# Optimization experiments

Measured on AMD Instinct MI355X. Metric: run time of the kernel, lower is better.

Reference implementation:

```python
import jax, jax.numpy as jnp
import numpy as np

N = 50000
E = 800000
IN_DIM = 128
HID = 64
HEADS = 4
OUT = 64


def _bn(x, g, b, eps=1e-5):
    # BatchNorm1d with batch statistics (biased var), as in train-mode normalization
    mu = x.mean(0)
    var = ((x - mu) ** 2).mean(0)
    return (x - mu) * jax.lax.rsqrt(var + eps) * g + b


def _gat(x, W, a_src, a_dst, bias, src, dst, heads, dim, concat):
    # PyG GATConv: h = xW; e_ij = LeakyReLU(a_src.h_j + a_dst.h_i); softmax over incoming edges of i
    n = x.shape[0]
    h = (x @ W).reshape(n, heads, dim)            # [N,H,D]
    es = (h * a_src).sum(-1)                      # [N,H]
    ed = (h * a_dst).sum(-1)                      # [N,H]
    e = jax.nn.leaky_relu(es[src] + ed[dst], 0.2)  # [E,H]
    emax = jax.ops.segment_max(e, dst, num_segments=n)
    w = jnp.exp(e - emax[dst])
    denom = jax.ops.segment_sum(w, dst, num_segments=n)
    alpha = w / (denom[dst] + 1e-16)              # [E,H]
    out = jax.ops.segment_sum(h[src] * alpha[:, :, None], dst, num_segments=n)  # [N,H,D]
    out = out.reshape(n, heads * dim) if concat else out.mean(axis=1)
    return out + bias


def _gcn(x, W, bias, src, dst):
    # PyG GCNConv with self-loops (already appended): D^{-1/2} A D^{-1/2} x W
    n = x.shape[0]
    h = x @ W
    deg = jax.ops.segment_sum(jnp.ones(src.shape[0], h.dtype), dst, num_segments=n)
    dinv = jax.lax.rsqrt(jnp.maximum(deg, 1e-12))
    norm = dinv[src] * dinv[dst]                  # [E]
    return jax.ops.segment_sum(h[src] * norm[:, None], dst, num_segments=n) + bias


def setup_inputs() -> dict:
    key = jax.random.key(0)
    ks = jax.random.split(key, 16)
    s = 0.1
    inp = {
        "x": jax.random.normal(ks[0], (N, IN_DIM), jnp.float32),
        "edge_index": jax.random.randint(ks[1], (2, E), 0, N, jnp.int64 if jax.config.jax_enable_x64 else jnp.int32),
        "edge_attr": jax.random.normal(ks[2], (E,), jnp.float32),
        # GAT layer 1
        "W1": jax.random.normal(ks[3], (IN_DIM, HEADS * HID), jnp.float32) * s,
        "att_src1": jax.random.normal(ks[4], (HEADS, HID), jnp.float32) * s,
        "att_dst1": jax.random.normal(ks[5], (HEADS, HID), jnp.float32) * s,
        "b1": jnp.zeros((HEADS * HID,), jnp.float32),
        "g1": jnp.ones((HEADS * HID,), jnp.float32),
        "beta1": jnp.zeros((HEADS * HID,), jnp.float32),
        # GCN
        "Wg": jax.random.normal(ks[6], (HEADS * HID, HID), jnp.float32) * s,
        "bg": jnp.zeros((HID,), jnp.float32),
        "g2": jnp.ones((HID,), jnp.float32),
        "beta2": jnp.zeros((HID,), jnp.float32),
        # GAT layer 2 (heads=1, concat=False)
        "W2": jax.random.normal(ks[7], (HID, OUT), jnp.float32) * s,
        "att_src2": jax.random.normal(ks[8], (1, OUT), jnp.float32) * s,
        "att_dst2": jax.random.normal(ks[9], (1, OUT), jnp.float32) * s,
        "b2": jnp.zeros((OUT,), jnp.float32),
        "g3": jnp.ones((OUT,), jnp.float32),
        "beta3": jnp.zeros((OUT,), jnp.float32),
        # projector
        "Wp1": jax.random.normal(ks[10], (OUT, 128), jnp.float32) * s,
        "bp1": jnp.zeros((128,), jnp.float32),
        "Wp2": jax.random.normal(ks[11], (128, 64), jnp.float32) * s,
        "bp2": jnp.zeros((64,), jnp.float32),
    }
    return inp


def reference(x, edge_index, edge_attr, W1, att_src1, att_dst1, b1, g1, beta1,
              Wg, bg, g2, beta2, W2, att_src2, att_dst2, b2, g3, beta3,
              Wp1, bp1, Wp2, bp2):
    # edge_attr is ignored by GATConv when edge_dim is None (PyG behavior)
    loop = jnp.arange(N, dtype=edge_index.dtype)
    src = jnp.concatenate([edge_index[0], loop])  # self-loops appended
    dst = jnp.concatenate([edge_index[1], loop])
    h = _gat(x, W1, att_src1, att_dst1, b1, src, dst, HEADS, HID, True)
    h = jax.nn.elu(_bn(h, g1, beta1))
    h = _gcn(h, Wg, bg, src, dst)
    h = jax.nn.relu(_bn(h, g2, beta2))
    h = _gat(h, W2, att_src2, att_dst2, b2, src, dst, 1, OUT, False)
    h = jax.nn.elu(_bn(h, g3, beta3))
    return jax.nn.relu(h @ Wp1 + bp1) @ Wp2 + bp2
```

## Files before the change

### kernel.cpp

```cpp
#include <hip/hip_runtime.h>
#include <math.h>

#define NN 50000
#define EE 800000
#define E2 850000
#define SCB 196
#define GXL 391

typedef __attribute__((ext_vector_type(8))) short short8;
typedef __attribute__((ext_vector_type(4))) float float4v;

__device__ __forceinline__ float bf2f(unsigned short u) {
  return __uint_as_float(((unsigned int)u) << 16);
}
__device__ __forceinline__ unsigned short f2bf(float f) {
  unsigned int x = __float_as_uint(f);
  unsigned int r = (x + 0x7fffu + ((x >> 16) & 1u)) >> 16;
  return (unsigned short)r;
}

__device__ __forceinline__ float leaky(float x) { return x > 0.f ? x : 0.2f * x; }

__device__ __forceinline__ int edge_src(const int* ei, int e) {
  return (e < EE) ? ei[e] : (e - EE);
}
__device__ __forceinline__ int edge_dst(const int* ei, int e) {
  return (e < EE) ? ei[EE + e] : (e - EE);
}

__global__ void k_deg(const int* __restrict__ ei, int* __restrict__ deg) {
  int e = blockIdx.x * blockDim.x + threadIdx.x;
  if (e < E2) atomicAdd(&deg[edge_dst(ei, e)], 1);
}

__global__ __launch_bounds__(256) void k_scan1(const int* __restrict__ deg,
                                               int* __restrict__ partial) {
  __shared__ int sd[256];
  int i = blockIdx.x * 256 + threadIdx.x;
  sd[threadIdx.x] = (i < NN) ? deg[i] : 0;
  __syncthreads();
  for (int off = 128; off > 0; off >>= 1) {
    if (threadIdx.x < off) sd[threadIdx.x] += sd[threadIdx.x + off];
    __syncthreads();
  }
  if (threadIdx.x == 0) partial[blockIdx.x] = sd[0];
}

__global__ __launch_bounds__(256) void k_scan3(const int* __restrict__ deg,
                                               const int* __restrict__ partial,
                                               int* __restrict__ rowptr,
                                               int* __restrict__ cnt,
                                               float* __restrict__ dinv) {
  __shared__ int sp[256];
  __shared__ int sd[256];
  int t = threadIdx.x;
  sp[t] = (t < SCB) ? partial[t] : 0;
  __syncthreads();
  for (int off = 1; off < 256; off <<= 1) {
    int v = (t >= off) ? sp[t - off] : 0;
    __syncthreads();
    sp[t] += v;
    __syncthreads();
  }
  int base = (blockIdx.x == 0) ? 0 : sp[blockIdx.x - 1];
  int i = blockIdx.x * 256 + t;
  int v = (i < NN) ? deg[i] : 0;
  sd[t] = v;
  __syncthreads();
  for (int off = 1; off < 256; off <<= 1) {
    int u = (t >= off) ? sd[t - off] : 0;
    __syncthreads();
    sd[t] += u;
    __syncthreads();
  }
  if (i < NN) {
    int excl = base + sd[t] - v;
    rowptr[i] = excl;
    cnt[i] = excl;
    dinv[i] = rsqrtf((float)v);
  }
  if (i == 0) rowptr[NN] = E2;
}

__global__ void k_fill(const int* __restrict__ ei, int* __restrict__ cnt,
                       int* __restrict__ csr) {
  int e = blockIdx.x * blockDim.x + threadIdx.x;
  if (e >= E2) return;
  int d = edge_dst(ei, e);
  int s = edge_src(ei, e);
  int pos = atomicAdd(&cnt[d], 1);
  csr[pos] = s;
}

template <int K, int ATTMODE, int INACT, bool ABF, bool USEBN>
__global__ __launch_bounds__(256) void k_gemm_mfma(
    const float* __restrict__ A, const unsigned short* __restrict__ Abf,
    const float* __restrict__ B, const float* __restrict__ biasOut,
    const float* __restrict__ bnst, const float* __restrict__ bng,
    const float* __restrict__ bnb, int outAct,
    float* __restrict__ Cf, unsigned short* __restrict__ Cbf,
    const float* __restrict__ rowScale,
    const float* __restrict__ attSrc, const float* __restrict__ attDst,
    float* __restrict__ esOut, float* __restrict__ edOut,
    int M, int NC) {
  __shared__ unsigned short BT[64][K + 8];
  __shared__ float sSc[256], sSh[256];
  int t = threadIdx.x;
  int lane = t & 63;
  int wv = t >> 6;
  int cl = lane & 15;
  int kg = lane >> 4;
  int rowBase = blockIdx.x * 128;
  int colBase = blockIdx.y * 64;

  if (USEBN) {
    int c = t;
    if (c < K) {
      float sum = 0.f, sq = 0.f;
      for (int cp = 0; cp < 32; ++cp) {
        sum += bnst[cp * 2 * K + c];
        sq += bnst[cp * 2 * K + K + c];
      }
      const float invN = 1.0f / (float)NN;
      float mu = sum * invN;
      float var = sq * invN - mu * mu;
      float rs = rsqrtf(var + 1e-5f);
      float sc = rs * bng[c];
      sSc[c] = sc;
      sSh[c] = fmaf(-mu, sc, bnb[c]);
    }
  }
  {
    int c = t & 63;
    for (int k = t >> 6; k < K; k += 4)
      BT[c][k] = f2bf(B[(size_t)k * NC + colBase + c]);
  }
  __syncthreads();

  float4v acc[2][4];
#pragma unroll
  for (int rt = 0; rt < 2; ++rt)
#pragma unroll
    for (int ct = 0; ct < 4; ++ct) acc[rt][ct] = (float4v){0.f, 0.f, 0.f, 0.f};

  int grA0 = rowBase + wv * 32 + cl;
  int grA1 = grA0 + 16;

#pragma unroll
  for (int kc = 0; kc < K; kc += 32) {
    int k0 = kc + kg * 8;
    short8 afr[2];
#pragma unroll
    for (int rt = 0; rt < 2; ++rt) {
      int gr = rt ? grA1 : grA0;
      float v[8];
      if (gr < M) {
        if (ABF) {
          ushort4 u0 = *(const ushort4*)&Abf[(size_t)gr * K + k0];
          ushort4 u1 = *(const ushort4*)&Abf[(size_t)gr * K + k0 + 4];
          v[0] = bf2f(u0.x); v[1] = bf2f(u0.y); v[2] = bf2f(u0.z); v[3] = bf2f(u0.w);
          v[4] = bf2f(u1.x); v[5] = bf2f(u1.y); v[6] = bf2f(u1.z); v[7] = bf2f(u1.w);
        } else {
          float4 f0 = *(const float4*)&A[(size_t)gr * K + k0];
          float4 f1 = *(const float4*)&A[(size_t)gr * K + k0 + 4];
          v[0] = f0.x; v[1] = f0.y; v[2] = f0.z; v[3] = f0.w;
          v[4] = f1.x; v[5] = f1.y; v[6] = f1.z; v[7] = f1.w;
        }
      } else {
#pragma unroll
        for (int i = 0; i < 8; ++i) v[i] = 0.f;
      }
#pragma unroll
      for (int i = 0; i < 8; ++i) {
        float x = v[i];
        if (USEBN) x = fmaf(x, sSc[k0 + i], sSh[k0 + i]);
        if (INACT == 1) x = fmaxf(x, 0.f);
        else if (INACT == 2) x = (x > 0.f) ? x : expm1f(x);
        afr[rt][i] = (short)f2bf(x);
      }
    }
    short8 bfr[4];
#pragma unroll
    for (int ct = 0; ct < 4; ++ct)
      bfr[ct] = *(const short8*)&BT[ct * 16 + cl][k0];
#pragma unroll
    for (int rt = 0; rt < 2; ++rt)
#pragma unroll
      for (int ct = 0; ct < 4; ++ct)
        acc[rt][ct] = __builtin_amdgcn_mfma_f32_16x16x32_bf16(
            afr[rt], bfr[ct], acc[rt][ct], 0, 0, 0);
  }

  float bb[4], as4[4], ad4[4];
#pragma unroll
  for (int ct = 0; ct < 4; ++ct) {
    int gc = colBase + ct * 16 + cl;
    bb[ct] = biasOut ? biasOut[gc] : 0.f;
    if (ATTMODE) {
      as4[ct] = attSrc[gc];
      ad4[ct] = attDst[gc];
    }
  }
#pragma unroll
  for (int rt = 0; rt < 2; ++rt) {
    float pes[4] = {0.f, 0.f, 0.f, 0.f};
    float ped[4] = {0.f, 0.f, 0.f, 0.f};
#pragma unroll
    for (int reg = 0; reg < 4; ++reg) {
      int gr = rowBase + wv * 32 + rt * 16 + kg * 4 + reg;
      bool ok = gr < M;
      float rs_ = 1.f;
      if (ok && Cbf && rowScale) rs_ = rowScale[gr];
#pragma unroll
      for (int ct = 0; ct < 4; ++ct) {
        float v = acc[rt][ct][reg] + bb[ct];
        if (outAct == 1) v = fmaxf(v, 0.f);
        int gc = colBase + ct * 16 + cl;
        if (ok) {
          if (Cf) Cf[(size_t)gr * NC + gc] = v;
          if (Cbf) Cbf[(size_t)gr * NC + gc] = f2bf(v * rs_);
        }
        if (ATTMODE) {
          pes[reg] = fmaf(v, as4[ct], pes[reg]);
          ped[reg] = fmaf(v, ad4[ct], ped[reg]);
        }
      }
    }
    if (ATTMODE) {
#pragma unroll
      for (int reg = 0; reg < 4; ++reg) {
#pragma unroll
        for (int off = 8; off > 0; off >>= 1) {
          pes[reg] += __shfl_xor(pes[reg], off);
          ped[reg] += __shfl_xor(ped[reg], off);
        }
      }
      if (cl == 0) {
#pragma unroll
        for (int reg = 0; reg < 4; ++reg) {
          int gr = rowBase + wv * 32 + rt * 16 + kg * 4 + reg;
          if (gr < M) {
            if (ATTMODE == 1) {
              esOut[gr * 4 + blockIdx.y] = pes[reg];
              edOut[gr * 4 + blockIdx.y] = ped[reg];
            } else {
              esOut[gr] = pes[reg];
              edOut[gr] = ped[reg];
            }
          }
        }
      }
    }
  }
}

__global__ __launch_bounds__(256) void k_soft1(const float* __restrict__ es,
                                               const float* __restrict__ ed,
                                               const int* __restrict__ rowptr,
                                               const int* __restrict__ csr,
                                               float* __restrict__ w1) {
  int node = blockIdx.x * 16 + (threadIdx.x >> 4);
  int sub = threadIdx.x & 15;
  int start = rowptr[node], end = rowptr[node + 1];
  float4 edv = *(const float4*)&ed[node * 4];
  float m0 = -1e30f, m1 = -1e30f, m2 = -1e30f, m3 = -1e30f;
  float s0 = 0.f, s1 = 0.f, s2 = 0.f, s3 = 0.f;
  for (int k = start + sub; k < end; k += 16) {
    int s = csr[k];
    float4 esv = *(const float4*)&es[s * 4];
    float e0 = leaky(esv.x + edv.x);
    float e1 = leaky(esv.y + edv.y);
    float e2 = leaky(esv.z + edv.z);
    float e3 = leaky(esv.w + edv.w);
    float mn;
    mn = fmaxf(m0, e0); s0 = s0 * __expf(m0 - mn) + __expf(e0 - mn); m0 = mn;
    mn = fmaxf(m1, e1); s1 = s1 * __expf(m1 - mn) + __expf(e1 - mn); m1 = mn;
    mn = fmaxf(m2, e2); s2 = s2 * __expf(m2 - mn) + __expf(e2 - mn); m2 = mn;
    mn = fmaxf(m3, e3); s3 = s3 * __expf(m3 - mn) + __expf(e3 - mn); m3 = mn;
  }
#pragma unroll
  for (int off = 1; off < 16; off <<= 1) {
    float mo, so, mn;
    mo = __shfl_xor(m0, off); so = __shfl_xor(s0, off);
    mn = fmaxf(m0, mo); s0 = s0 * __expf(m0 - mn) + so * __expf(mo - mn); m0 = mn;
    mo = __shfl_xor(m1, off); so = __shfl_xor(s1, off);
    mn = fmaxf(m1, mo); s1 = s1 * __expf(m1 - mn) + so * __expf(mo - mn); m1 = mn;
    mo = __shfl_xor(m2, off); so = __shfl_xor(s2, off);
    mn = fmaxf(m2, mo); s2 = s2 * __expf(m2 - mn) + so * __expf(mo - mn); m2 = mn;
    mo = __shfl_xor(m3, off); so = __shfl_xor(s3, off);
    mn = fmaxf(m3, mo); s3 = s3 * __expf(m3 - mn) + so * __expf(mo - mn); m3 = mn;
  }
  float i0 = 1.f / (s0 + 1e-16f);
  float i1 = 1.f / (s1 + 1e-16f);
  float i2 = 1.f / (s2 + 1e-16f);
  float i3 = 1.f / (s3 + 1e-16f);
  for (int k = start + sub; k < end; k += 16) {
    int s = csr[k];
    float4 esv = *(const float4*)&es[s * 4];
    w1[k]          = __expf(leaky(esv.x + edv.x) - m0) * i0;
    w1[E2 + k]     = __expf(leaky(esv.y + edv.y) - m1) * i1;
    w1[2 * E2 + k] = __expf(leaky(esv.z + edv.z) - m2) * i2;
    w1[3 * E2 + k] = __expf(leaky(esv.w + edv.w) - m3) * i3;
  }
}

__global__ __launch_bounds__(256) void k_soft2(const float* __restrict__ es,
                                               const float* __restrict__ ed,
                                               const int* __restrict__ rowptr,
                                               const int* __restrict__ csr,
                                               float* __restrict__ w2) {
  int node = blockIdx.x * 16 + (threadIdx.x >> 4);
  int sub = threadIdx.x & 15;
  int start = rowptr[node], end = rowptr[node + 1];
  float edi = ed[node];
  float m = -1e30f, ss = 0.f;
  for (int k = start + sub; k < end; k += 16) {
    float e = leaky(es[csr[k]] + edi);
    float mn = fmaxf(m, e);
    ss = ss * __expf(m - mn) + __expf(e - mn);
    m = mn;
  }
#pragma unroll
  for (int off = 1; off < 16; off <<= 1) {
    float mo = __shfl_xor(m, off);
    float so = __shfl_xor(ss, off);
    float mn = fmaxf(m, mo);
    ss = ss * __expf(m - mn) + so * __expf(mo - mn);
    m = mn;
  }
  float inv = 1.f / (ss + 1e-16f);
  for (int k = start + sub; k < end; k += 16) {
    float e = leaky(es[csr[k]] + edi);
    w2[k] = __expf(e - m) * inv;
  }
}

__global__ __launch_bounds__(256) void k_gat1(const unsigned short* __restrict__ h1b,
                                              const float* __restrict__ w1,
                                              const int* __restrict__ rowptr,
                                              const int* __restrict__ csr,
                                              const float* __restrict__ b1,
                                              unsigned short* __restrict__ outb,
                                              float* __restrict__ st) {
  __shared__ float smS[4][256];
  __shared__ float smQ[4][256];
  int wave = threadIdx.x >> 6;
  int lane = threadIdx.x & 63;
  int i = blockIdx.x * 4 + wave;
  int start = rowptr[i], end = rowptr[i + 1];
  const float* wh = w1 + (size_t)(lane >> 4) * E2;
  float4 acc = make_float4(0.f, 0.f, 0.f, 0.f);
  int k = start;
  for (; k + 4 <= end; k += 4) {
    int sA = csr[k], sB = csr[k + 1], sC = csr[k + 2], sD = csr[k + 3];
    float wA = wh[k], wB = wh[k + 1], wC = wh[k + 2], wD = wh[k + 3];
    ushort4 a0 = *(const ushort4*)&h1b[(size_t)sA * 256 + lane * 4];
    ushort4 a1 = *(const ushort4*)&h1b[(size_t)sB * 256 + lane * 4];
    ushort4 a2 = *(const ushort4*)&h1b[(size_t)sC * 256 + lane * 4];
    ushort4 a3 = *(const ushort4*)&h1b[(size_t)sD * 256 + lane * 4];
    acc.x = fmaf(bf2f(a0.x), wA, fmaf(bf2f(a1.x), wB, fmaf(bf2f(a2.x), wC, fmaf(bf2f(a3.x), wD, acc.x))));
    acc.y = fmaf(bf2f(a0.y), wA, fmaf(bf2f(a1.y), wB, fmaf(bf2f(a2.y), wC, fmaf(bf2f(a3.y), wD, acc.y))));
    acc.z = fmaf(bf2f(a0.z), wA, fmaf(bf2f(a1.z), wB, fmaf(bf2f(a2.z), wC, fmaf(bf2f(a3.z), wD, acc.z))));
    acc.w = fmaf(bf2f(a0.w), wA, fmaf(bf2f(a1.w), wB, fmaf(bf2f(a2.w), wC, fmaf(bf2f(a3.w), wD, acc.w))));
  }
  for (; k < end; ++k) {
    int s = csr[k];
    float wv = wh[k];
    ushort4 a0 = *(const ushort4*)&h1b[(size_t)s * 256 + lane * 4];
    acc.x = fmaf(bf2f(a0.x), wv, acc.x);
    acc.y = fmaf(bf2f(a0.y), wv, acc.y);
    acc.z = fmaf(bf2f(a0.z), wv, acc.z);
    acc.w = fmaf(bf2f(a0.w), wv, acc.w);
  }
  float4 bv = *(const float4*)&b1[lane * 4];
  float4 o;
  o.x = acc.x + bv.x; o.y = acc.y + bv.y; o.z = acc.z + bv.z; o.w = acc.w + bv.w;
  ushort4 u;
  u.x = f2bf(o.x); u.y = f2bf(o.y); u.z = f2bf(o.z); u.w = f2bf(o.w);
  *(ushort4*)&outb[(size_t)i * 256 + lane * 4] = u;
  *(float4*)&smS[wave][lane * 4] = o;
  float4 q = make_float4(o.x * o.x, o.y * o.y, o.z * o.z, o.w * o.w);
  *(float4*)&smQ[wave][lane * 4] = q;
  __syncthreads();
  int c = threadIdx.x;
  float s_ = 0.f, q_ = 0.f;
#pragma unroll
  for (int wv = 0; wv < 4; ++wv) { s_ += smS[wv][c]; q_ += smQ[wv][c]; }
  float* dst = st + (size_t)(blockIdx.x & 31) * 512;
  atomicAdd(&dst[c], s_);
  atomicAdd(&dst[256 + c], q_);
}

__global__ __launch_bounds__(256) void k_gcn(const unsigned short* __restrict__ hgb,
                                             const float* __restrict__ dinv,
                                             const int* __restrict__ rowptr,
                                             const int* __restrict__ csr,
                                             const float* __restrict__ bg,
                                             float* __restrict__ out,
                                             float* __restrict__ st) {
  __shared__ float2 sm[4][64];
  int wave = threadIdx.x >> 6;
  int lane = threadIdx.x & 63;
  int i = blockIdx.x * 4 + wave;
  int start = rowptr[i], end = rowptr[i + 1];
  float acc = 0.f;
  int k = start;
  for (; k + 4 <= end; k += 4) {
    int sA = csr[k], sB = csr[k + 1], sC = csr[k + 2], sD = csr[k + 3];
    acc += bf2f(hgb[(size_t)sA * 64 + lane]) + bf2f(hgb[(size_t)sB * 64 + lane]) +
           bf2f(hgb[(size_t)sC * 64 + lane]) + bf2f(hgb[(size_t)sD * 64 + lane]);
  }
  for (; k < end; ++k) acc += bf2f(hgb[(size_t)csr[k] * 64 + lane]);
  float o = fmaf(acc, dinv[i], bg[lane]);
  out[(size_t)i * 64 + lane] = o;
  sm[wave][lane] = make_float2(o, o * o);
  __syncthreads();
  if (threadIdx.x < 64) {
    int c = threadIdx.x;
    float s_ = 0.f, q_ = 0.f;
#pragma unroll
    for (int wv = 0; wv < 4; ++wv) { float2 v = sm[wv][c]; s_ += v.x; q_ += v.y; }
    float* dst = st + (size_t)(blockIdx.x & 31) * 128;
    atomicAdd(&dst[c], s_);
    atomicAdd(&dst[64 + c], q_);
  }
}

__global__ __launch_bounds__(256) void k_gat2(const unsigned short* __restrict__ h2b,
                                              const float* __restrict__ w2,
                                              const int* __restrict__ rowptr,
                                              const int* __restrict__ csr,
                                              const float* __restrict__ b2,
                                              float* __restrict__ out,
                                              float* __restrict__ st) {
  __shared__ float2 sm[4][64];
  int wave = threadIdx.x >> 6;
  int lane = threadIdx.x & 63;
  int i = blockIdx.x * 4 + wave;
  int start = rowptr[i], end = rowptr[i + 1];
  float acc = 0.f;
  int k = start;
  for (; k + 4 <= end; k += 4) {
    int sA = csr[k], sB = csr[k + 1], sC = csr[k + 2], sD = csr[k + 3];
    float wA = w2[k], wB = w2[k + 1], wC = w2[k + 2], wD = w2[k + 3];
    acc = fmaf(bf2f(h2b[(size_t)sA * 64 + lane]), wA,
          fmaf(bf2f(h2b[(size_t)sB * 64 + lane]), wB,
          fmaf(bf2f(h2b[(size_t)sC * 64 + lane]), wC,
          fmaf(bf2f(h2b[(size_t)sD * 64 + lane]), wD, acc))));
  }
  for (; k < end; ++k)
    acc = fmaf(bf2f(h2b[(size_t)csr[k] * 64 + lane]), w2[k], acc);
  float o = acc + b2[lane];
  out[(size_t)i * 64 + lane] = o;
  sm[wave][lane] = make_float2(o, o * o);
  __syncthreads();
  if (threadIdx.x < 64) {
    int c = threadIdx.x;
    float s_ = 0.f, q_ = 0.f;
#pragma unroll
    for (int wv = 0; wv < 4; ++wv) { float2 v = sm[wv][c]; s_ += v.x; q_ += v.y; }
    float* dst = st + (size_t)(blockIdx.x & 31) * 128;
    atomicAdd(&dst[c], s_);
    atomicAdd(&dst[64 + c], q_);
  }
}

extern "C" void kernel_launch(void* const* d_in, const int* in_sizes, int n_in,
                              void* d_out, int out_size, void* d_ws, size_t ws_size,
                              hipStream_t stream) {
  const float* x        = (const float*)d_in[0];
  const int*   ei       = (const int*)d_in[1];
  const float* W1       = (const float*)d_in[3];
  const float* att_src1 = (const float*)d_in[4];
  const float* att_dst1 = (const float*)d_in[5];
  const float* b1       = (const float*)d_in[6];
  const float* g1       = (const float*)d_in[7];
  const float* beta1    = (const float*)d_in[8];
  const float* Wg       = (const float*)d_in[9];
  const float* bg       = (const float*)d_in[10];
  const float* g2       = (const float*)d_in[11];
  const float* beta2    = (const float*)d_in[12];
  const float* W2       = (const float*)d_in[13];
  const float* att_src2 = (const float*)d_in[14];
  const float* att_dst2 = (const float*)d_in[15];
  const float* b2       = (const float*)d_in[16];
  const float* g3       = (const float*)d_in[17];
  const float* beta3    = (const float*)d_in[18];
  const float* Wp1      = (const float*)d_in[19];
  const float* bp1      = (const float*)d_in[20];
  const float* Wp2      = (const float*)d_in[21];
  const float* bp2      = (const float*)d_in[22];
  float* out = (float*)d_out;

  char* w = (char*)d_ws;
  unsigned short* bufBb  = (unsigned short*)(w + 0);
  float*          bufD   = (float*)(w + 0);
  unsigned short* h1b    = (unsigned short*)(w + 51200000);
  float*          hidden = (float*)(w + 51200000);
  float*          w1     = (float*)(w + 76800000);
  float*          w2     = (float*)(w + 76800000);
  unsigned short* hgb    = (unsigned short*)(w + 90400000);
  float*          bufC   = (float*)(w + 96800000);
  unsigned short* h2b    = (unsigned short*)(w + 109600000);
  float*          es1    = (float*)(w + 116000000);
  float*          ed1    = (float*)(w + 116800000);
  float*          es2    = (float*)(w + 117600000);
  float*          ed2    = (float*)(w + 117800000);
  float*          dinv   = (float*)(w + 118000000);
  int*            deg    = (int*)(w + 118200000);
  int*            rowptr = (int*)(w + 118400000);
  int*            cnt    = (int*)(w + 118600064);
  int*            csr    = (int*)(w + 118800064);
  float*          st1    = (float*)(w + 122200064);
  float*          st2    = st1 + 32 * 512;
  float*          st3    = st2 + 32 * 128;
  int*            partial= (int*)(st3 + 32 * 128);

  hipMemsetAsync(deg, 0, NN * sizeof(int), stream);
  hipMemsetAsync(st1, 0, (32 * 512 + 32 * 128 + 32 * 128) * sizeof(float), stream);

  const int EB = (E2 + 255) / 256;
  const int WB = NN / 4;
  const int SB = NN / 16;

  k_deg<<<EB, 256, 0, stream>>>(ei, deg);
  k_scan1<<<SCB, 256, 0, stream>>>(deg, partial);
  k_scan3<<<SCB, 256, 0, stream>>>(deg, partial, rowptr, cnt, dinv);
  k_fill<<<EB, 256, 0, stream>>>(ei, cnt, csr);

  k_gemm_mfma<128, 1, 0, false, false><<<dim3(GXL, 4), 256, 0, stream>>>(
      x, nullptr, W1, nullptr, nullptr, nullptr, nullptr, 0,
      nullptr, h1b, nullptr, att_src1, att_dst1, es1, ed1, NN, 256);
  k_soft1<<<SB, 256, 0, stream>>>(es1, ed1, rowptr, csr, w1);
  k_gat1<<<WB, 256, 0, stream>>>(h1b, w1, rowptr, csr, b1, bufBb, st1);

  k_gemm_mfma<256, 0, 2, true, true><<<dim3(GXL, 1), 256, 0, stream>>>(
      nullptr, bufBb, Wg, nullptr, st1, g1, beta1, 0,
      nullptr, hgb, dinv, nullptr, nullptr, nullptr, nullptr, NN, 64);
  k_gcn<<<WB, 256, 0, stream>>>(hgb, dinv, rowptr, csr, bg, bufC, st2);

  k_gemm_mfma<64, 2, 1, false, true><<<dim3(GXL, 1), 256, 0, stream>>>(
      bufC, nullptr, W2, nullptr, st2, g2, beta2, 0,
      nullptr, h2b, nullptr, att_src2, att_dst2, es2, ed2, NN, 64);
  k_soft2<<<SB, 256, 0, stream>>>(es2, ed2, rowptr, csr, w2);
  k_gat2<<<WB, 256, 0, stream>>>(h2b, w2, rowptr, csr, b2, bufD, st3);

  k_gemm_mfma<64, 0, 2, false, true><<<dim3(GXL, 2), 256, 0, stream>>>(
      bufD, nullptr, Wp1, bp1, st3, g3, beta3, 1,
      hidden, nullptr, nullptr, nullptr, nullptr, nullptr, nullptr, NN, 128);
  k_gemm_mfma<128, 0, 0, false, false><<<dim3(GXL, 1), 256, 0, stream>>>(
      hidden, nullptr, Wp2, bp2, nullptr, nullptr, nullptr, 0,
      out, nullptr, nullptr, nullptr, nullptr, nullptr, nullptr, NN, 64);
}
```

Measured before the change: 485.4 us.

## Add fused GEMM1 kernel, widen gather loads, store intermediates in bf16

A dedicated first-layer GEMM is added. It loads each A tile once and loops over the four column groups, where the old kernel launched four column blocks that each re-read x. The GAT1, GCN and GAT2 aggregation kernels now use 16-byte bf16 vector loads, split edges across sub-groups of lanes and combine them with cross-lane shuffles. GCN, GAT2 and projector-hidden outputs are stored as bf16 instead of fp32, and the later GEMMs read bf16 inputs, which cuts memory traffic at the cost of some precision.

```diff
diff --git a/kernel.cpp b/kernel.cpp
--- a/kernel.cpp
+++ b/kernel.cpp
@@ -8,6 +8,7 @@
 #define GXL 391
 
 typedef __attribute__((ext_vector_type(8))) short short8;
+typedef __attribute__((ext_vector_type(8))) unsigned short ushort8v;
 typedef __attribute__((ext_vector_type(4))) float float4v;
 
 __device__ __forceinline__ float bf2f(unsigned short u) {
@@ -90,6 +91,118 @@
   int s = edge_src(ei, e);
   int pos = atomicAdd(&cnt[d], 1);
   csr[pos] = s;
+}
+
+__global__ __launch_bounds__(256) void k_gemm1(
+    const float* __restrict__ A, const float* __restrict__ B,
+    unsigned short* __restrict__ Cbf,
+    const float* __restrict__ attSrc, const float* __restrict__ attDst,
+    float* __restrict__ esOut, float* __restrict__ edOut, int M) {
+  __shared__ unsigned short BT[64][136];
+  int t = threadIdx.x;
+  int lane = t & 63;
+  int wv = t >> 6;
+  int cl = lane & 15;
+  int kg = lane >> 4;
+  int rowBase = blockIdx.x * 128;
+
+  short8 afr[2][4];
+  int grA0 = rowBase + wv * 32 + cl;
+#pragma unroll
+  for (int rt = 0; rt < 2; ++rt) {
+    int gr = grA0 + rt * 16;
+#pragma unroll
+    for (int ks = 0; ks < 4; ++ks) {
+      int k0 = ks * 32 + kg * 8;
+      if (gr < M) {
+        float4 f0 = *(const float4*)&A[(size_t)gr * 128 + k0];
+        float4 f1 = *(const float4*)&A[(size_t)gr * 128 + k0 + 4];
+        afr[rt][ks][0] = (short)f2bf(f0.x); afr[rt][ks][1] = (short)f2bf(f0.y);
+        afr[rt][ks][2] = (short)f2bf(f0.z); afr[rt][ks][3] = (short)f2bf(f0.w);
+        afr[rt][ks][4] = (short)f2bf(f1.x); afr[rt][ks][5] = (short)f2bf(f1.y);
+        afr[rt][ks][6] = (short)f2bf(f1.z); afr[rt][ks][7] = (short)f2bf(f1.w);
+      } else {
+#pragma unroll
+        for (int j = 0; j < 8; ++j) afr[rt][ks][j] = 0;
+      }
+    }
+  }
+
+  for (int cg = 0; cg < 4; ++cg) {
+    int colBase = cg * 64;
+    {
+      int c = t & 63;
+      for (int k = t >> 6; k < 128; k += 4)
+        BT[c][k] = f2bf(B[(size_t)k * 256 + colBase + c]);
+    }
+    __syncthreads();
+
+    float4v acc[2][4];
+#pragma unroll
+    for (int rt = 0; rt < 2; ++rt)
+#pragma unroll
+      for (int ct = 0; ct < 4; ++ct) acc[rt][ct] = (float4v){0.f, 0.f, 0.f, 0.f};
+
+#pragma unroll
+    for (int ks = 0; ks < 4; ++ks) {
+      int k0 = ks * 32 + kg * 8;
+      short8 bfr[4];
+#pragma unroll
+      for (int ct = 0; ct < 4; ++ct)
+        bfr[ct] = *(const short8*)&BT[ct * 16 + cl][k0];
+#pragma unroll
+      for (int rt = 0; rt < 2; ++rt)
+#pragma unroll
+        for (int ct = 0; ct < 4; ++ct)
+          acc[rt][ct] = __builtin_amdgcn_mfma_f32_16x16x32_bf16(
+              afr[rt][ks], bfr[ct], acc[rt][ct], 0, 0, 0);
+    }
+
+    float as4[4], ad4[4];
+#pragma unroll
+    for (int ct = 0; ct < 4; ++ct) {
+      int gc = colBase + ct * 16 + cl;
+      as4[ct] = attSrc[gc];
+      ad4[ct] = attDst[gc];
+    }
+#pragma unroll
+    for (int rt = 0; rt < 2; ++rt) {
+      float pes[4] = {0.f, 0.f, 0.f, 0.f};
+      float ped[4] = {0.f, 0.f, 0.f, 0.f};
+#pragma unroll
+      for (int reg = 0; reg < 4; ++reg) {
+        int gr = rowBase + wv * 32 + rt * 16 + kg * 4 + reg;
+        bool ok = gr < M;
+#pragma unroll
+        for (int ct = 0; ct < 4; ++ct) {
+          float v = acc[rt][ct][reg];
+          int gc = colBase + ct * 16 + cl;
+          if (ok) Cbf[(size_t)gr * 256 + gc] = f2bf(v);
+          pes[reg] = fmaf(v, as4[ct], pes[reg]);
+          ped[reg] = fmaf(v, ad4[ct], ped[reg]);
+        }
+      }
+#pragma unroll
+      for (int reg = 0; reg < 4; ++reg) {
+#pragma unroll
+        for (int off = 8; off > 0; off >>= 1) {
+          pes[reg] += __shfl_xor(pes[reg], off);
+          ped[reg] += __shfl_xor(ped[reg], off);
+        }
+      }
+      if (cl == 0) {
+#pragma unroll
+        for (int reg = 0; reg < 4; ++reg) {
+          int gr = rowBase + wv * 32 + rt * 16 + kg * 4 + reg;
+          if (gr < M) {
+            esOut[gr * 4 + cg] = pes[reg];
+            edOut[gr * 4 + cg] = ped[reg];
+          }
+        }
+      }
+    }
+    __syncthreads();
+  }
 }
 
 template <int K, int ATTMODE, int INACT, bool ABF, bool USEBN>
@@ -348,39 +461,66 @@
   int lane = threadIdx.x & 63;
   int i = blockIdx.x * 4 + wave;
   int start = rowptr[i], end = rowptr[i + 1];
-  const float* wh = w1 + (size_t)(lane >> 4) * E2;
-  float4 acc = make_float4(0.f, 0.f, 0.f, 0.f);
+  int half = lane >> 5;
+  int cl5 = lane & 31;
+  int head = cl5 >> 3;
+  int cOff = cl5 * 8;
+  const float* wh = w1 + (size_t)head * E2;
+  float acc[8];
+#pragma unroll
+  for (int j = 0; j < 8; ++j) acc[j] = 0.f;
+
   int k = start;
   for (; k + 4 <= end; k += 4) {
-    int sA = csr[k], sB = csr[k + 1], sC = csr[k + 2], sD = csr[k + 3];
-    float wA = wh[k], wB = wh[k + 1], wC = wh[k + 2], wD = wh[k + 3];
-    ushort4 a0 = *(const ushort4*)&h1b[(size_t)sA * 256 + lane * 4];
-    ushort4 a1 = *(const ushort4*)&h1b[(size_t)sB * 256 + lane * 4];
-    ushort4 a2 = *(const ushort4*)&h1b[(size_t)sC * 256 + lane * 4];
-    ushort4 a3 = *(const ushort4*)&h1b[(size_t)sD * 256 + lane * 4];
-    acc.x = fmaf(bf2f(a0.x), wA, fmaf(bf2f(a1.x), wB, fmaf(bf2f(a2.x), wC, fmaf(bf2f(a3.x), wD, acc.x))));
-    acc.y = fmaf(bf2f(a0.y), wA, fmaf(bf2f(a1.y), wB, fmaf(bf2f(a2.y), wC, fmaf(bf2f(a3.y), wD, acc.y))));
-    acc.z = fmaf(bf2f(a0.z), wA, fmaf(bf2f(a1.z), wB, fmaf(bf2f(a2.z), wC, fmaf(bf2f(a3.z), wD, acc.z))));
-    acc.w = fmaf(bf2f(a0.w), wA, fmaf(bf2f(a1.w), wB, fmaf(bf2f(a2.w), wC, fmaf(bf2f(a3.w), wD, acc.w))));
-  }
-  for (; k < end; ++k) {
+#pragma unroll
+    for (int u = 0; u < 2; ++u) {
+      int kk = k + u * 2 + half;
+      int s = csr[kk];
+      float wv = wh[kk];
+      ushort8v hv = *(const ushort8v*)&h1b[(size_t)s * 256 + cOff];
+#pragma unroll
+      for (int j = 0; j < 8; ++j) acc[j] = fmaf(bf2f(hv[j]), wv, acc[j]);
+    }
+  }
+  for (; k + 2 <= end; k += 2) {
+    int kk = k + half;
+    int s = csr[kk];
+    float wv = wh[kk];
+    ushort8v hv = *(const ushort8v*)&h1b[(size_t)s * 256 + cOff];
+#pragma unroll
+    for (int j = 0; j < 8; ++j) acc[j] = fmaf(bf2f(hv[j]), wv, acc[j]);
+  }
+  if (k < end) {
     int s = csr[k];
-    float wv = wh[k];
-    ushort4 a0 = *(const ushort4*)&h1b[(size_t)s * 256 + lane * 4];
-    acc.x = fmaf(bf2f(a0.x), wv, acc.x);
-    acc.y = fmaf(bf2f(a0.y), wv, acc.y);
-    acc.z = fmaf(bf2f(a0.z), wv, acc.z);
-    acc.w = fmaf(bf2f(a0.w), wv, acc.w);
-  }
-  float4 bv = *(const float4*)&b1[lane * 4];
-  float4 o;
-  o.x = acc.x + bv.x; o.y = acc.y + bv.y; o.z = acc.z + bv.z; o.w = acc.w + bv.w;
-  ushort4 u;
-  u.x = f2bf(o.x); u.y = f2bf(o.y); u.z = f2bf(o.z); u.w = f2bf(o.w);
-  *(ushort4*)&outb[(size_t)i * 256 + lane * 4] = u;
-  *(float4*)&smS[wave][lane * 4] = o;
-  float4 q = make_float4(o.x * o.x, o.y * o.y, o.z * o.z, o.w * o.w);
-  *(float4*)&smQ[wave][lane * 4] = q;
+    float wv = (half == 0) ? wh[k] : 0.f;
+    ushort8v hv = *(const ushort8v*)&h1b[(size_t)s * 256 + cOff];
+#pragma unroll
+    for (int j = 0; j < 8; ++j) acc[j] = fmaf(bf2f(hv[j]), wv, acc[j]);
+  }
+#pragma unroll
+  for (int j = 0; j < 8; ++j) acc[j] += __shfl_xor(acc[j], 32);
+
+  float4 b0 = *(const float4*)&b1[cOff];
+  float4 b1v = *(const float4*)&b1[cOff + 4];
+  float bb[8] = {b0.x, b0.y, b0.z, b0.w, b1v.x, b1v.y, b1v.z, b1v.w};
+  if (half == 0) {
+    float o[8];
+    ushort8v u8;
+#pragma unroll
+    for (int j = 0; j < 8; ++j) {
+      o[j] = acc[j] + bb[j];
+      u8[j] = f2bf(o[j]);
+    }
+    *(ushort8v*)&outb[(size_t)i * 256 + cOff] = u8;
+    float4 s0 = make_float4(o[0], o[1], o[2], o[3]);
+    float4 s1 = make_float4(o[4], o[5], o[6], o[7]);
+    *(float4*)&smS[wave][cOff] = s0;
+    *(float4*)&smS[wave][cOff + 4] = s1;
+    float4 q0 = make_float4(o[0]*o[0], o[1]*o[1], o[2]*o[2], o[3]*o[3]);
+    float4 q1 = make_float4(o[4]*o[4], o[5]*o[5], o[6]*o[6], o[7]*o[7]);
+    *(float4*)&smQ[wave][cOff] = q0;
+    *(float4*)&smQ[wave][cOff + 4] = q1;
+  }
   __syncthreads();
   int c = threadIdx.x;
   float s_ = 0.f, q_ = 0.f;
@@ -396,30 +536,63 @@
                                              const int* __restrict__ rowptr,
                                              const int* __restrict__ csr,
                                              const float* __restrict__ bg,
-                                             float* __restrict__ out,
+                                             unsigned short* __restrict__ outb,
                                              float* __restrict__ st) {
-  __shared__ float2 sm[4][64];
+  __shared__ float smS[4][64];
+  __shared__ float smQ[4][64];
   int wave = threadIdx.x >> 6;
   int lane = threadIdx.x & 63;
   int i = blockIdx.x * 4 + wave;
   int start = rowptr[i], end = rowptr[i + 1];
-  float acc = 0.f;
+  int grp = lane >> 3;
+  int cOff = (lane & 7) * 8;
+  float acc[8];
+#pragma unroll
+  for (int j = 0; j < 8; ++j) acc[j] = 0.f;
+
   int k = start;
-  for (; k + 4 <= end; k += 4) {
-    int sA = csr[k], sB = csr[k + 1], sC = csr[k + 2], sD = csr[k + 3];
-    acc += bf2f(hgb[(size_t)sA * 64 + lane]) + bf2f(hgb[(size_t)sB * 64 + lane]) +
-           bf2f(hgb[(size_t)sC * 64 + lane]) + bf2f(hgb[(size_t)sD * 64 + lane]);
-  }
-  for (; k < end; ++k) acc += bf2f(hgb[(size_t)csr[k] * 64 + lane]);
-  float o = fmaf(acc, dinv[i], bg[lane]);
-  out[(size_t)i * 64 + lane] = o;
-  sm[wave][lane] = make_float2(o, o * o);
+  for (; k + 8 <= end; k += 8) {
+    int s = csr[k + grp];
+    ushort8v hv = *(const ushort8v*)&hgb[(size_t)s * 64 + cOff];
+#pragma unroll
+    for (int j = 0; j < 8; ++j) acc[j] += bf2f(hv[j]);
+  }
+  if (k < end) {
+    int kk = k + grp;
+    bool act = kk < end;
+    int s = csr[act ? kk : start];
+    float m_ = act ? 1.f : 0.f;
+    ushort8v hv = *(const ushort8v*)&hgb[(size_t)s * 64 + cOff];
+#pragma unroll
+    for (int j = 0; j < 8; ++j) acc[j] = fmaf(bf2f(hv[j]), m_, acc[j]);
+  }
+#pragma unroll
+  for (int off = 8; off <= 32; off <<= 1)
+#pragma unroll
+    for (int j = 0; j < 8; ++j) acc[j] += __shfl_xor(acc[j], off);
+
+  if (lane < 8) {
+    float di = dinv[i];
+    float4 g0 = *(const float4*)&bg[cOff];
+    float4 g1 = *(const float4*)&bg[cOff + 4];
+    float bb[8] = {g0.x, g0.y, g0.z, g0.w, g1.x, g1.y, g1.z, g1.w};
+    float o[8];
+    ushort8v u8;
+#pragma unroll
+    for (int j = 0; j < 8; ++j) {
+      o[j] = fmaf(acc[j], di, bb[j]);
+      u8[j] = f2bf(o[j]);
+      smS[wave][cOff + j] = o[j];
+      smQ[wave][cOff + j] = o[j] * o[j];
+    }
+    *(ushort8v*)&outb[(size_t)i * 64 + cOff] = u8;
+  }
   __syncthreads();
   if (threadIdx.x < 64) {
     int c = threadIdx.x;
     float s_ = 0.f, q_ = 0.f;
 #pragma unroll
-    for (int wv = 0; wv < 4; ++wv) { float2 v = sm[wv][c]; s_ += v.x; q_ += v.y; }
+    for (int wv = 0; wv < 4; ++wv) { s_ += smS[wv][c]; q_ += smQ[wv][c]; }
     float* dst = st + (size_t)(blockIdx.x & 31) * 128;
     atomicAdd(&dst[c], s_);
     atomicAdd(&dst[64 + c], q_);
@@ -431,34 +604,64 @@
                                               const int* __restrict__ rowptr,
                                               const int* __restrict__ csr,
                                               const float* __restrict__ b2,
-                                              float* __restrict__ out,
+                                              unsigned short* __restrict__ outb,
                                               float* __restrict__ st) {
-  __shared__ float2 sm[4][64];
+  __shared__ float smS[4][64];
+  __shared__ float smQ[4][64];
   int wave = threadIdx.x >> 6;
   int lane = threadIdx.x & 63;
   int i = blockIdx.x * 4 + wave;
   int start = rowptr[i], end = rowptr[i + 1];
-  float acc = 0.f;
+  int grp = lane >> 3;
+  int cOff = (lane & 7) * 8;
+  float acc[8];
+#pragma unroll
+  for (int j = 0; j < 8; ++j) acc[j] = 0.f;
+
   int k = start;
-  for (; k + 4 <= end; k += 4) {
-    int sA = csr[k], sB = csr[k + 1], sC = csr[k + 2], sD = csr[k + 3];
-    float wA = w2[k], wB = w2[k + 1], wC = w2[k + 2], wD = w2[k + 3];
-    acc = fmaf(bf2f(h2b[(size_t)sA * 64 + lane]), wA,
-          fmaf(bf2f(h2b[(size_t)sB * 64 + lane]), wB,
-          fmaf(bf2f(h2b[(size_t)sC * 64 + lane]), wC,
-          fmaf(bf2f(h2b[(size_t)sD * 64 + lane]), wD, acc))));
-  }
-  for (; k < end; ++k)
-    acc = fmaf(bf2f(h2b[(size_t)csr[k] * 64 + lane]), w2[k], acc);
-  float o = acc + b2[lane];
-  out[(size_t)i * 64 + lane] = o;
-  sm[wave][lane] = make_float2(o, o * o);
+  for (; k + 8 <= end; k += 8) {
+    int kk = k + grp;
+    int s = csr[kk];
+    float wv = w2[kk];
+    ushort8v hv = *(const ushort8v*)&h2b[(size_t)s * 64 + cOff];
+#pragma unroll
+    for (int j = 0; j < 8; ++j) acc[j] = fmaf(bf2f(hv[j]), wv, acc[j]);
+  }
+  if (k < end) {
+    int kk = k + grp;
+    bool act = kk < end;
+    int s = csr[act ? kk : start];
+    float wv = act ? w2[kk] : 0.f;
+    ushort8v hv = *(const ushort8v*)&h2b[(size_t)s * 64 + cOff];
+#pragma unroll
+    for (int j = 0; j < 8; ++j) acc[j] = fmaf(bf2f(hv[j]), wv, acc[j]);
+  }
+#pragma unroll
+  for (int off = 8; off <= 32; off <<= 1)
+#pragma unroll
+    for (int j = 0; j < 8; ++j) acc[j] += __shfl_xor(acc[j], off);
+
+  if (lane < 8) {
+    float4 g0 = *(const float4*)&b2[cOff];
+    float4 g1 = *(const float4*)&b2[cOff + 4];
+    float bb[8] = {g0.x, g0.y, g0.z, g0.w, g1.x, g1.y, g1.z, g1.w};
+    float o[8];
+    ushort8v u8;
+#pragma unroll
+    for (int j = 0; j < 8; ++j) {
+      o[j] = acc[j] + bb[j];
+      u8[j] = f2bf(o[j]);
+      smS[wave][cOff + j] = o[j];
+      smQ[wave][cOff + j] = o[j] * o[j];
+    }
+    *(ushort8v*)&outb[(size_t)i * 64 + cOff] = u8;
+  }
   __syncthreads();
   if (threadIdx.x < 64) {
     int c = threadIdx.x;
     float s_ = 0.f, q_ = 0.f;
 #pragma unroll
-    for (int wv = 0; wv < 4; ++wv) { float2 v = sm[wv][c]; s_ += v.x; q_ += v.y; }
+    for (int wv = 0; wv < 4; ++wv) { s_ += smS[wv][c]; q_ += smQ[wv][c]; }
     float* dst = st + (size_t)(blockIdx.x & 31) * 128;
     atomicAdd(&dst[c], s_);
     atomicAdd(&dst[64 + c], q_);
@@ -494,13 +697,13 @@
 
   char* w = (char*)d_ws;
   unsigned short* bufBb  = (unsigned short*)(w + 0);
-  float*          bufD   = (float*)(w + 0);
+  unsigned short* bufDb  = (unsigned short*)(w + 0);
   unsigned short* h1b    = (unsigned short*)(w + 51200000);
-  float*          hidden = (float*)(w + 51200000);
+  unsigned short* hiddenb= (unsigned short*)(w + 51200000);
   float*          w1     = (float*)(w + 76800000);
   float*          w2     = (float*)(w + 76800000);
   unsigned short* hgb    = (unsigned short*)(w + 90400000);
-  float*          bufC   = (float*)(w + 96800000);
+  unsigned short* bufCb  = (unsigned short*)(w + 96800000);
   unsigned short* h2b    = (unsigned short*)(w + 109600000);
   float*          es1    = (float*)(w + 116000000);
   float*          ed1    = (float*)(w + 116800000);
@@ -528,27 +731,25 @@
   k_scan3<<<SCB, 256, 0, stream>>>(deg, partial, rowptr, cnt, dinv);
   k_fill<<<EB, 256, 0, stream>>>(ei, cnt, csr);
 
-  k_gemm_mfma<128, 1, 0, false, false><<<dim3(GXL, 4), 256, 0, stream>>>(
-      x, nullptr, W1, nullptr, nullptr, nullptr, nullptr, 0,
-      nullptr, h1b, nullptr, att_src1, att_dst1, es1, ed1, NN, 256);
+  k_gemm1<<<GXL, 256, 0, stream>>>(x, W1, h1b, att_src1, att_dst1, es1, ed1, NN);
   k_soft1<<<SB, 256, 0, stream>>>(es1, ed1, rowptr, csr, w1);
   k_gat1<<<WB, 256, 0, stream>>>(h1b, w1, rowptr, csr, b1, bufBb, st1);
 
   k_gemm_mfma<256, 0, 2, true, true><<<dim3(GXL, 1), 256, 0, stream>>>(
       nullptr, bufBb, Wg, nullptr, st1, g1, beta1, 0,
       nullptr, hgb, dinv, nullptr, nullptr, nullptr, nullptr, NN, 64);
-  k_gcn<<<WB, 256, 0, stream>>>(hgb, dinv, rowptr, csr, bg, bufC, st2);
-
-  k_gemm_mfma<64, 2, 1, false, true><<<dim3(GXL, 1), 256, 0, stream>>>(
-      bufC, nullptr, W2, nullptr, st2, g2, beta2, 0,
+  k_gcn<<<WB, 256, 0, stream>>>(hgb, dinv, rowptr, csr, bg, bufCb, st2);
+
+  k_gemm_mfma<64, 2, 1, true, true><<<dim3(GXL, 1), 256, 0, stream>>>(
+      nullptr, bufCb, W2, nullptr, st2, g2, beta2, 0,
       nullptr, h2b, nullptr, att_src2, att_dst2, es2, ed2, NN, 64);
   k_soft2<<<SB, 256, 0, stream>>>(es2, ed2, rowptr, csr, w2);
-  k_gat2<<<WB, 256, 0, stream>>>(h2b, w2, rowptr, csr, b2, bufD, st3);
-
-  k_gemm_mfma<64, 0, 2, false, true><<<dim3(GXL, 2), 256, 0, stream>>>(
-      bufD, nullptr, Wp1, bp1, st3, g3, beta3, 1,
-      hidden, nullptr, nullptr, nullptr, nullptr, nullptr, nullptr, NN, 128);
-  k_gemm_mfma<128, 0, 0, false, false><<<dim3(GXL, 1), 256, 0, stream>>>(
-      hidden, nullptr, Wp2, bp2, nullptr, nullptr, nullptr, 0,
+  k_gat2<<<WB, 256, 0, stream>>>(h2b, w2, rowptr, csr, b2, bufDb, st3);
+
+  k_gemm_mfma<64, 0, 2, true, true><<<dim3(GXL, 2), 256, 0, stream>>>(
+      nullptr, bufDb, Wp1, bp1, st3, g3, beta3, 1,
+      nullptr, hiddenb, nullptr, nullptr, nullptr, nullptr, nullptr, NN, 128);
+  k_gemm_mfma<128, 0, 0, true, false><<<dim3(GXL, 1), 256, 0, stream>>>(
+      nullptr, hiddenb, Wp2, bp2, nullptr, nullptr, nullptr, 0,
       out, nullptr, nullptr, nullptr, nullptr, nullptr, nullptr, NN, 64);
 }
```

Result: faster. 450.0 us (-7.3%).
